# Kernel optimization log

Hardware: AMD Instinct MI355X
Metric: run time of the kernel (lower is better)

The kernel has to match this reference:

```python
import jax, jax.numpy as jnp
import numpy as np

N = 50000   # nodes
E = 600000  # edges
D = 128     # embedding_dim
L = 4       # num_message_passing_steps


def setup_inputs() -> dict:
    key = jax.random.key(0)
    ks = jax.random.split(key, 5)
    x = jax.random.normal(ks[0], (N, D), dtype=jnp.float32)
    edge_index = jax.random.randint(ks[1], (2, E), 0, N, dtype=jnp.int32)
    # Per-layer params: MPNN linear (no bias), GCNConv weight + bias.
    lin_w = jax.random.normal(ks[2], (L, D, D), dtype=jnp.float32) / np.sqrt(D).astype(np.float32)
    gcn_w = jax.random.normal(ks[3], (L, D, D), dtype=jnp.float32) / np.sqrt(D).astype(np.float32)
    gcn_b = jax.random.normal(ks[4], (L, D), dtype=jnp.float32) * 0.01
    return {"x": x, "edge_index": edge_index, "lin_w": lin_w, "gcn_w": gcn_w, "gcn_b": gcn_b}


def reference(x, edge_index, lin_w, gcn_w, gcn_b):
    n = x.shape[0]
    # GCNConv defaults: add_self_loops=True, normalize=True.
    loops = jnp.arange(n, dtype=edge_index.dtype)
    src = jnp.concatenate([edge_index[0], loops])  # [E+N]
    dst = jnp.concatenate([edge_index[1], loops])  # [E+N]
    # Degree computed on dst (col) for flow='source_to_target'.
    deg = jax.ops.segment_sum(jnp.ones_like(src, dtype=x.dtype), dst, num_segments=n)
    dinv = jnp.where(deg > 0, jax.lax.rsqrt(jnp.maximum(deg, 1.0)), 0.0)
    norm = dinv[src] * dinv[dst]  # [E+N]

    for l in range(lin_w.shape[0]):
        h = x @ lin_w[l].T                 # MPNNLayer.linear (no bias)
        h = h @ gcn_w[l].T                 # GCNConv internal linear
        msgs = h[src] * norm[:, None]      # gather + normalize  [E+N, D]
        agg = jax.ops.segment_sum(msgs, dst, num_segments=n)
        x = agg + gcn_b[l]                 # GCNConv bias
        # NOTE: self.relu is `Sequential as ReLU` -> empty Sequential = identity.
    return x
```

## Files before the change

### kernel.cpp

```cpp
#include <hip/hip_runtime.h>

#define DEMB 128

typedef __attribute__((ext_vector_type(8))) _Float16 half8;
typedef __attribute__((ext_vector_type(4))) _Float16 half4;
typedef __attribute__((ext_vector_type(4))) float f32x4;

__global__ void kwc(const float* __restrict__ gcn, const float* __restrict__ lin,
                    float* __restrict__ Ms) {
  __shared__ float sa[128];
  int l = blockIdx.x >> 7, i = blockIdx.x & 127, j = threadIdx.x;
  sa[j] = gcn[((size_t)l * 128 + i) * 128 + j];
  __syncthreads();
  float acc = 0.f;
#pragma unroll 8
  for (int k = 0; k < 128; ++k) acc += sa[k] * lin[((size_t)l * 128 + k) * 128 + j];
  Ms[((size_t)l * 128 + i) * 128 + j] = acc;
}

__global__ void kst2(const float* __restrict__ Ms, const float* __restrict__ gb,
                     float* __restrict__ A1, float* __restrict__ B1,
                     float* __restrict__ v0, float* __restrict__ cb) {
  const float* M0 = Ms;
  const float* M1 = Ms + 16384;
  const float* M2 = Ms + 2 * 16384;
  const float* M3 = Ms + 3 * 16384;
  __shared__ float sa[128];
  int b = blockIdx.x, j = threadIdx.x;
  if (b < 128) {
    sa[j] = M1[b * 128 + j];
    __syncthreads();
    float acc = 0.f;
#pragma unroll 8
    for (int k = 0; k < 128; ++k) acc += sa[k] * M0[k * 128 + j];
    A1[b * 128 + j] = acc;
  } else if (b < 256) {
    int i = b - 128;
    sa[j] = M3[i * 128 + j];
    __syncthreads();
    float acc = 0.f;
#pragma unroll 8
    for (int k = 0; k < 128; ++k) acc += sa[k] * M2[k * 128 + j];
    B1[i * 128 + j] = acc;
  } else if (b == 256) {
    sa[j] = gb[j];
    __syncthreads();
    float acc = 0.f;
#pragma unroll 8
    for (int k = 0; k < 128; ++k) acc += M1[j * 128 + k] * sa[k];
    v0[j] = acc;
  } else {
    sa[j] = gb[2 * 128 + j];
    __syncthreads();
    float acc = 0.f;
#pragma unroll 8
    for (int k = 0; k < 128; ++k) acc += M3[j * 128 + k] * sa[k];
    cb[256 + j] = acc;
  }
}

__global__ void kst3(const float* __restrict__ A1, const float* __restrict__ B1,
                     const float* __restrict__ v0, const float* __restrict__ gb,
                     _Float16* __restrict__ Rh, float* __restrict__ cb) {
  __shared__ float sa[128];
  int b = blockIdx.x, j = threadIdx.x;
  if (b < 128) {
    sa[j] = B1[b * 128 + j];
    __syncthreads();
    float acc = 0.f;
#pragma unroll 8
    for (int k = 0; k < 128; ++k) acc += sa[k] * A1[k * 128 + j];
    Rh[b * 128 + j] = (_Float16)acc;
  } else if (b == 128) {
    sa[j] = v0[j];
    __syncthreads();
    float acc = 0.f;
#pragma unroll 8
    for (int k = 0; k < 128; ++k) acc += B1[j * 128 + k] * sa[k];
    cb[j] = acc;
  } else {
    sa[j] = gb[128 + j];
    __syncthreads();
    float acc = 0.f;
#pragma unroll 8
    for (int k = 0; k < 128; ++k) acc += B1[j * 128 + k] * sa[k];
    cb[128 + j] = acc;
  }
}

__global__ void kdeg(const int* __restrict__ ei, int* __restrict__ deg, int etot) {
  int i = blockIdx.x * 256 + threadIdx.x;
  if (i < etot) atomicAdd(&deg[ei[etot + i]], 1);
}

__global__ void kscan1(const int* __restrict__ deg, int* __restrict__ off,
                       int* __restrict__ bsum, float* __restrict__ dinv,
                       float* __restrict__ dinv2, int n) {
  __shared__ int s[256];
  int t = threadIdx.x, i = blockIdx.x * 256 + t;
  int c = 0;
  if (i < n) {
    c = deg[i];
    float dv = rsqrtf((float)(c + 1));
    dinv[i] = dv;
    dinv2[i] = dv * dv;
  }
  s[t] = c;
  __syncthreads();
  for (int o = 1; o < 256; o <<= 1) {
    int v = (t >= o) ? s[t - o] : 0;
    __syncthreads();
    s[t] += v;
    __syncthreads();
  }
  if (i < n) off[i] = s[t] - c;
  if (t == 255) bsum[blockIdx.x] = s[t];
}

__global__ void kscan2(const int* __restrict__ bsum, int* __restrict__ boff,
                       int nb, int* __restrict__ off, int n, int etot) {
  __shared__ int s[256];
  int t = threadIdx.x;
  int c = (t < nb) ? bsum[t] : 0;
  s[t] = c;
  __syncthreads();
  for (int o = 1; o < 256; o <<= 1) {
    int v = (t >= o) ? s[t - o] : 0;
    __syncthreads();
    s[t] += v;
    __syncthreads();
  }
  if (t < nb) boff[t] = s[t] - c;
  if (t == 0) off[n] = etot;
}

__global__ void kscan3(int* __restrict__ off, const int* __restrict__ boff,
                       int* __restrict__ cur, int n) {
  int i = blockIdx.x * 256 + threadIdx.x;
  if (i < n) {
    int o = off[i] + boff[i >> 8];
    off[i] = o;
    cur[i] = o;
  }
}

__global__ void kfill(const int* __restrict__ ei, int* __restrict__ cur,
                      int* __restrict__ csr, int etot) {
  int i = blockIdx.x * 256 + threadIdx.x;
  if (i < etot) {
    int d = ei[etot + i];
    int p = atomicAdd(&cur[d], 1);
    csr[p] = ei[i];
  }
}

__global__ void kpre(const float* __restrict__ x, const float* __restrict__ dinv,
                     _Float16* __restrict__ xh, int n) {
  int gid = blockIdx.x * 256 + threadIdx.x;
  if (gid >= n * 32) return;
  int r = gid >> 5, c = (gid & 31) * 4;
  float d = dinv[r];
  float4 v = *(const float4*)(x + (size_t)r * DEMB + c);
  half4 o = {(_Float16)(v.x * d), (_Float16)(v.y * d), (_Float16)(v.z * d), (_Float16)(v.w * d)};
  *(half4*)(xh + (size_t)r * DEMB + c) = o;
}

template <int WITHU>
__launch_bounds__(256, 8)
__global__ void kagg16(const _Float16* __restrict__ vin, const int* __restrict__ csr,
                       const int* __restrict__ off, const float* __restrict__ scale,
                       const float* __restrict__ dinv, const float* __restrict__ a_in,
                       float* __restrict__ u_out, float* __restrict__ a_out,
                       _Float16* __restrict__ vout, int n) {
  int node = (int)((blockIdx.x * 256u + threadIdx.x) >> 4);
  if (node >= n) return;
  int l16 = threadIdx.x & 15;
  const _Float16* base = vin + 8 * l16;
  half8 sv = *(const half8*)(base + (size_t)node * DEMB);
  float acc[8];
#pragma unroll
  for (int j = 0; j < 8; ++j) acc[j] = (float)sv[j];
  float s = WITHU ? a_in[node] : 0.f;
  int e = off[node], end = off[node + 1];
  for (; e + 8 <= end; e += 8) {
    int i0 = csr[e], i1 = csr[e + 1], i2 = csr[e + 2], i3 = csr[e + 3];
    int i4 = csr[e + 4], i5 = csr[e + 5], i6 = csr[e + 6], i7 = csr[e + 7];
    half8 r0 = *(const half8*)(base + (size_t)i0 * DEMB);
    half8 r1 = *(const half8*)(base + (size_t)i1 * DEMB);
    half8 r2 = *(const half8*)(base + (size_t)i2 * DEMB);
    half8 r3 = *(const half8*)(base + (size_t)i3 * DEMB);
    half8 r4 = *(const half8*)(base + (size_t)i4 * DEMB);
    half8 r5 = *(const half8*)(base + (size_t)i5 * DEMB);
    half8 r6 = *(const half8*)(base + (size_t)i6 * DEMB);
    half8 r7 = *(const half8*)(base + (size_t)i7 * DEMB);
    if (WITHU)
      s += a_in[i0] + a_in[i1] + a_in[i2] + a_in[i3] +
           a_in[i4] + a_in[i5] + a_in[i6] + a_in[i7];
#pragma unroll
    for (int j = 0; j < 8; ++j)
      acc[j] += ((float)r0[j] + (float)r1[j]) + ((float)r2[j] + (float)r3[j]) +
                ((float)r4[j] + (float)r5[j]) + ((float)r6[j] + (float)r7[j]);
  }
  for (; e + 4 <= end; e += 4) {
    int i0 = csr[e], i1 = csr[e + 1], i2 = csr[e + 2], i3 = csr[e + 3];
    half8 r0 = *(const half8*)(base + (size_t)i0 * DEMB);
    half8 r1 = *(const half8*)(base + (size_t)i1 * DEMB);
    half8 r2 = *(const half8*)(base + (size_t)i2 * DEMB);
    half8 r3 = *(const half8*)(base + (size_t)i3 * DEMB);
    if (WITHU) s += a_in[i0] + a_in[i1] + a_in[i2] + a_in[i3];
#pragma unroll
    for (int j = 0; j < 8; ++j)
      acc[j] += ((float)r0[j] + (float)r1[j]) + ((float)r2[j] + (float)r3[j]);
  }
  if (e < end) {
    int em = end - 1;
    int i0 = csr[e];
    int i1 = csr[min(e + 1, em)];
    int i2 = csr[min(e + 2, em)];
    float w1 = (e + 1 < end) ? 1.f : 0.f;
    float w2 = (e + 2 < end) ? 1.f : 0.f;
    half8 r0 = *(const half8*)(base + (size_t)i0 * DEMB);
    half8 r1 = *(const half8*)(base + (size_t)i1 * DEMB);
    half8 r2 = *(const half8*)(base + (size_t)i2 * DEMB);
    if (WITHU) s += a_in[i0] + w1 * a_in[i1] + w2 * a_in[i2];
#pragma unroll
    for (int j = 0; j < 8; ++j)
      acc[j] += (float)r0[j] + w1 * (float)r1[j] + w2 * (float)r2[j];
  }
  float sc = scale[node];
  half8 o;
#pragma unroll
  for (int j = 0; j < 8; ++j) o[j] = (_Float16)(acc[j] * sc);
  *(half8*)(vout + (size_t)node * DEMB + 8 * l16) = o;
  if (WITHU && l16 == 0) {
    float dv = dinv[node];
    float u = dv * s;
    u_out[node] = u;
    a_out[node] = dv * u;
  }
}

__launch_bounds__(256)
__global__ void kgemm16(const _Float16* __restrict__ y, const _Float16* __restrict__ Rh,
                        const float* __restrict__ u1, const float* __restrict__ u2,
                        const float* __restrict__ u3, const float* __restrict__ cb,
                        const float* __restrict__ b3, float* __restrict__ out, int n) {
  int t = threadIdx.x;
  int wv = t >> 6, lane = t & 63;
  int l16 = lane & 15, g = lane >> 4;
  int row0 = blockIdx.x * 128 + wv * 32;
  f32x4 acc[2][8];
#pragma unroll
  for (int w = 0; w < 2; ++w)
#pragma unroll
    for (int n8 = 0; n8 < 8; ++n8) acc[w][n8] = (f32x4){0.f, 0.f, 0.f, 0.f};

#pragma unroll
  for (int k0 = 0; k0 < 128; k0 += 32) {
    half8 a0 = *(const half8*)(y + (size_t)(row0 + l16) * DEMB + k0 + g * 8);
    half8 a1 = *(const half8*)(y + (size_t)(row0 + 16 + l16) * DEMB + k0 + g * 8);
#pragma unroll
    for (int n8 = 0; n8 < 8; ++n8) {
      half8 b = *(const half8*)(Rh + (size_t)(n8 * 16 + l16) * DEMB + k0 + g * 8);
      acc[0][n8] = __builtin_amdgcn_mfma_f32_16x16x32_f16(a0, b, acc[0][n8], 0, 0, 0);
      acc[1][n8] = __builtin_amdgcn_mfma_f32_16x16x32_f16(a1, b, acc[1][n8], 0, 0, 0);
    }
  }
#pragma unroll
  for (int n8 = 0; n8 < 8; ++n8) {
    int col = n8 * 16 + l16;
    float cA = cb[col], cB = cb[128 + col], cC = cb[256 + col], bb = b3[col];
#pragma unroll
    for (int w = 0; w < 2; ++w)
#pragma unroll
      for (int r = 0; r < 4; ++r) {
        int row = row0 + w * 16 + g * 4 + r;
        if (row < n) {
          out[(size_t)row * DEMB + col] =
              acc[w][n8][r] + u3[row] * cA + u2[row] * cB + u1[row] * cC + bb;
        }
      }
  }
}

extern "C" void kernel_launch(void* const* d_in, const int* in_sizes, int n_in,
                              void* d_out, int out_size, void* d_ws, size_t ws_size,
                              hipStream_t stream) {
  const float* x0 = (const float*)d_in[0];
  const int* ei = (const int*)d_in[1];
  const float* lin = (const float*)d_in[2];
  const float* gcn = (const float*)d_in[3];
  const float* gb = (const float*)d_in[4];
  float* out = (float*)d_out;

  int N = in_sizes[0] / DEMB;
  int E = in_sizes[1] / 2;
  int L = in_sizes[2] / (DEMB * DEMB);
  int NP = (N + 127) & ~127;

  char* w = (char*)d_ws;
  auto carve = [&](size_t bytes) {
    char* p = w;
    w += (bytes + 255) & ~(size_t)255;
    return p;
  };
  float* Ms    = (float*)carve((size_t)L * DEMB * DEMB * 4);
  float* A1    = (float*)carve((size_t)DEMB * DEMB * 4);
  float* B1    = (float*)carve((size_t)DEMB * DEMB * 4);
  _Float16* Rh = (_Float16*)carve((size_t)DEMB * DEMB * 2);
  float* v0    = (float*)carve((size_t)DEMB * 4);
  float* cb    = (float*)carve((size_t)3 * DEMB * 4);
  float* dinv  = (float*)carve((size_t)N * 4);
  float* dnv2  = (float*)carve((size_t)N * 4);
  int* deg     = (int*)carve((size_t)N * 4);
  int* off     = (int*)carve((size_t)(N + 1) * 4);
  int* cur     = (int*)carve((size_t)N * 4);
  int* bsum    = (int*)carve(256 * 4);
  int* boff    = (int*)carve(256 * 4);
  int* csr     = (int*)carve((size_t)E * 4);
  float* u1    = (float*)carve((size_t)N * 4);
  float* u2    = (float*)carve((size_t)N * 4);
  float* u3    = (float*)carve((size_t)N * 4);
  float* a1    = (float*)carve((size_t)N * 4);
  float* a2    = (float*)carve((size_t)N * 4);
  float* a3    = (float*)carve((size_t)N * 4);
  _Float16* ha = (_Float16*)carve((size_t)NP * DEMB * 2);
  _Float16* hb = (_Float16*)carve((size_t)NP * DEMB * 2);
  (void)ws_size; (void)n_in; (void)out_size;

  int nbN = (N + 255) / 256;
  int nbE = (E + 255) / 256;
  int nbA = (N * 16 + 255) / 256;

  hipMemsetAsync(deg, 0, (size_t)N * 4, stream);

  kwc<<<L * DEMB, DEMB, 0, stream>>>(gcn, lin, Ms);
  kst2<<<258, DEMB, 0, stream>>>(Ms, gb, A1, B1, v0, cb);
  kst3<<<130, DEMB, 0, stream>>>(A1, B1, v0, gb, Rh, cb);

  kdeg<<<nbE, 256, 0, stream>>>(ei, deg, E);
  kscan1<<<nbN, 256, 0, stream>>>(deg, off, bsum, dinv, dnv2, N);
  kscan2<<<1, 256, 0, stream>>>(bsum, boff, nbN, off, N, E);
  kscan3<<<nbN, 256, 0, stream>>>(off, boff, cur, N);
  kfill<<<nbE, 256, 0, stream>>>(ei, cur, csr, E);

  kpre<<<(N * 32 + 255) / 256, 256, 0, stream>>>(x0, dinv, ha, N);
  kagg16<1><<<nbA, 256, 0, stream>>>(ha, csr, off, dnv2, dinv, dinv, u1, a1, hb, N);
  kagg16<1><<<nbA, 256, 0, stream>>>(hb, csr, off, dnv2, dinv, a1, u2, a2, ha, N);
  kagg16<1><<<nbA, 256, 0, stream>>>(ha, csr, off, dnv2, dinv, a2, u3, a3, hb, N);
  kagg16<0><<<nbA, 256, 0, stream>>>(hb, csr, off, dinv, dinv, nullptr, nullptr, nullptr, ha, N);

  kgemm16<<<(N + 127) / 128, 256, 0, stream>>>(ha, Rh, u1, u2, u3, cb, gb + 3 * DEMB, out, N);
}
```

Before: 233.3 us.

## Build CSR via two-level binned counting sort with shared-memory atomics

Replaces the global-atomic degree count and global-atomic CSR fill with a two-pass bucket sort. Edges are first binned by dst>>8 using per-block shared-memory histograms, a prefix over bins, and a scatter into a (src,dst) pair buffer. Per-bin kernels then compute degrees and fill the CSR with shared-memory atomics. This removes contended global atomics and scattered writes, at the cost of extra kernels, an 8-byte-per-edge intermediate buffer and a single-block serial base computation. It also drops the occupancy hint on the aggregation kernel.

```diff
diff --git a/kernel.cpp b/kernel.cpp
--- a/kernel.cpp
+++ b/kernel.cpp
@@ -1,6 +1,7 @@
 #include <hip/hip_runtime.h>
 
 #define DEMB 128
+#define EB 8192
 
 typedef __attribute__((ext_vector_type(8))) _Float16 half8;
 typedef __attribute__((ext_vector_type(4))) _Float16 half4;
@@ -88,9 +89,77 @@
   }
 }
 
-__global__ void kdeg(const int* __restrict__ ei, int* __restrict__ deg, int etot) {
-  int i = blockIdx.x * 256 + threadIdx.x;
-  if (i < etot) atomicAdd(&deg[ei[etot + i]], 1);
+__global__ void khist(const int* __restrict__ ei, int* __restrict__ histG,
+                      int etot, int nbB) {
+  __shared__ int lh[256];
+  int t = threadIdx.x;
+  lh[t] = 0;
+  __syncthreads();
+#pragma unroll 4
+  for (int j = 0; j < EB / 256; ++j) {
+    int i = blockIdx.x * EB + j * 256 + t;
+    if (i < etot) atomicAdd(&lh[ei[etot + i] >> 8], 1);
+  }
+  __syncthreads();
+  histG[t * nbB + blockIdx.x] = lh[t];
+}
+
+__global__ void kbase(int* __restrict__ histG, int* __restrict__ binOff,
+                      int nbB, int etot) {
+  __shared__ int s[256];
+  int t = threadIdx.x;
+  int* row = histG + t * nbB;
+  int tot = 0;
+#pragma unroll 4
+  for (int b = 0; b < nbB; ++b) tot += row[b];
+  s[t] = tot;
+  __syncthreads();
+  for (int o = 1; o < 256; o <<= 1) {
+    int v = (t >= o) ? s[t - o] : 0;
+    __syncthreads();
+    s[t] += v;
+    __syncthreads();
+  }
+  int bstart = s[t] - tot;
+  binOff[t] = bstart;
+  if (t == 255) binOff[256] = etot;
+  int run = bstart;
+  for (int b = 0; b < nbB; ++b) {
+    int v = row[b];
+    row[b] = run;
+    run += v;
+  }
+}
+
+__global__ void kscatter(const int* __restrict__ ei, const int* __restrict__ histG,
+                         int2* __restrict__ pr, int etot, int nbB) {
+  __shared__ int cur[256];
+  int t = threadIdx.x;
+  cur[t] = histG[t * nbB + blockIdx.x];
+  __syncthreads();
+#pragma unroll 4
+  for (int j = 0; j < EB / 256; ++j) {
+    int i = blockIdx.x * EB + j * 256 + t;
+    if (i < etot) {
+      int src = ei[i], dst = ei[etot + i];
+      int p = atomicAdd(&cur[dst >> 8], 1);
+      pr[p] = make_int2(src, dst);
+    }
+  }
+}
+
+__global__ void kdeg2(const int2* __restrict__ pr, const int* __restrict__ binOff,
+                      int* __restrict__ deg, int n) {
+  __shared__ int dl[256];
+  int t = threadIdx.x, b = blockIdx.x;
+  dl[t] = 0;
+  __syncthreads();
+  int s1 = binOff[b + 1];
+  for (int p = binOff[b] + t; p < s1; p += 256)
+    atomicAdd(&dl[pr[p].y & 255], 1);
+  __syncthreads();
+  int node = (b << 8) + t;
+  if (node < n) deg[node] = dl[t];
 }
 
 __global__ void kscan1(const int* __restrict__ deg, int* __restrict__ off,
@@ -134,23 +203,23 @@
   if (t == 0) off[n] = etot;
 }
 
-__global__ void kscan3(int* __restrict__ off, const int* __restrict__ boff,
-                       int* __restrict__ cur, int n) {
+__global__ void kscan3(int* __restrict__ off, const int* __restrict__ boff, int n) {
   int i = blockIdx.x * 256 + threadIdx.x;
-  if (i < n) {
-    int o = off[i] + boff[i >> 8];
-    off[i] = o;
-    cur[i] = o;
-  }
-}
-
-__global__ void kfill(const int* __restrict__ ei, int* __restrict__ cur,
-                      int* __restrict__ csr, int etot) {
-  int i = blockIdx.x * 256 + threadIdx.x;
-  if (i < etot) {
-    int d = ei[etot + i];
-    int p = atomicAdd(&cur[d], 1);
-    csr[p] = ei[i];
+  if (i < n) off[i] += boff[i >> 8];
+}
+
+__global__ void kfill2(const int2* __restrict__ pr, const int* __restrict__ binOff,
+                       const int* __restrict__ off, int* __restrict__ csr, int n) {
+  __shared__ int cur[256];
+  int t = threadIdx.x, b = blockIdx.x;
+  int node = (b << 8) + t;
+  cur[t] = (node < n) ? off[node] : 0;
+  __syncthreads();
+  int s1 = binOff[b + 1];
+  for (int p = binOff[b] + t; p < s1; p += 256) {
+    int2 e = pr[p];
+    int pos = atomicAdd(&cur[e.y & 255], 1);
+    csr[pos] = e.x;
   }
 }
 
@@ -166,7 +235,7 @@
 }
 
 template <int WITHU>
-__launch_bounds__(256, 8)
+__launch_bounds__(256)
 __global__ void kagg16(const _Float16* __restrict__ vin, const int* __restrict__ csr,
                        const int* __restrict__ off, const float* __restrict__ scale,
                        const float* __restrict__ dinv, const float* __restrict__ a_in,
@@ -297,6 +366,8 @@
   int E = in_sizes[1] / 2;
   int L = in_sizes[2] / (DEMB * DEMB);
   int NP = (N + 127) & ~127;
+  int NBINS = (N + 255) >> 8;
+  int nbB = (E + EB - 1) / EB;
 
   char* w = (char*)d_ws;
   auto carve = [&](size_t bytes) {
@@ -314,7 +385,9 @@
   float* dnv2  = (float*)carve((size_t)N * 4);
   int* deg     = (int*)carve((size_t)N * 4);
   int* off     = (int*)carve((size_t)(N + 1) * 4);
-  int* cur     = (int*)carve((size_t)N * 4);
+  int* histG   = (int*)carve((size_t)256 * nbB * 4);
+  int* binOff  = (int*)carve(257 * 4);
+  int2* pr     = (int2*)carve((size_t)E * 8);
   int* bsum    = (int*)carve(256 * 4);
   int* boff    = (int*)carve(256 * 4);
   int* csr     = (int*)carve((size_t)E * 4);
@@ -329,22 +402,22 @@
   (void)ws_size; (void)n_in; (void)out_size;
 
   int nbN = (N + 255) / 256;
-  int nbE = (E + 255) / 256;
-  int nbA = (N * 16 + 255) / 256;
-
-  hipMemsetAsync(deg, 0, (size_t)N * 4, stream);
 
   kwc<<<L * DEMB, DEMB, 0, stream>>>(gcn, lin, Ms);
   kst2<<<258, DEMB, 0, stream>>>(Ms, gb, A1, B1, v0, cb);
   kst3<<<130, DEMB, 0, stream>>>(A1, B1, v0, gb, Rh, cb);
 
-  kdeg<<<nbE, 256, 0, stream>>>(ei, deg, E);
+  khist<<<nbB, 256, 0, stream>>>(ei, histG, E, nbB);
+  kbase<<<1, 256, 0, stream>>>(histG, binOff, nbB, E);
+  kscatter<<<nbB, 256, 0, stream>>>(ei, histG, pr, E, nbB);
+  kdeg2<<<NBINS, 256, 0, stream>>>(pr, binOff, deg, N);
   kscan1<<<nbN, 256, 0, stream>>>(deg, off, bsum, dinv, dnv2, N);
   kscan2<<<1, 256, 0, stream>>>(bsum, boff, nbN, off, N, E);
-  kscan3<<<nbN, 256, 0, stream>>>(off, boff, cur, N);
-  kfill<<<nbE, 256, 0, stream>>>(ei, cur, csr, E);
+  kscan3<<<nbN, 256, 0, stream>>>(off, boff, N);
+  kfill2<<<NBINS, 256, 0, stream>>>(pr, binOff, off, csr, N);
 
   kpre<<<(N * 32 + 255) / 256, 256, 0, stream>>>(x0, dinv, ha, N);
+  int nbA = (N * 16 + 255) / 256;
   kagg16<1><<<nbA, 256, 0, stream>>>(ha, csr, off, dnv2, dinv, dinv, u1, a1, hb, N);
   kagg16<1><<<nbA, 256, 0, stream>>>(hb, csr, off, dnv2, dinv, a1, u2, a2, ha, N);
   kagg16<1><<<nbA, 256, 0, stream>>>(ha, csr, off, dnv2, dinv, a2, u3, a3, hb, N);
```

Result: faster. 220.0 us (-5.7%).
